# Performance work log

Hardware: AMD Instinct MI355X
Metric: run time of the kernel (lower is better)

Reference implementation:

```python
import jax, jax.numpy as jnp
import numpy as np

N_EMBD = 1024
HEAD_SIZE = 128

def setup_inputs() -> dict:
    key = jax.random.key(0)
    k1, k2, k3, k4 = jax.random.split(key, 4)
    x = jax.random.normal(k1, (8, 2048, N_EMBD), dtype=jnp.float32)
    # Linear(n_embd, head_size, bias=False): y = x @ W, W: [n_embd, head_size]
    s = 1.0 / np.sqrt(N_EMBD)
    Wk = jax.random.uniform(k2, (N_EMBD, HEAD_SIZE), jnp.float32, -s, s)
    Wq = jax.random.uniform(k3, (N_EMBD, HEAD_SIZE), jnp.float32, -s, s)
    Wv = jax.random.uniform(k4, (N_EMBD, HEAD_SIZE), jnp.float32, -s, s)
    return {"x": x, "Wk": Wk, "Wq": Wq, "Wv": Wv}

def reference(x, Wk, Wq, Wv):
    B, T, C = x.shape
    H = Wk.shape[1]
    k = jnp.einsum('btc,ch->bth', x, Wk)
    q = jnp.einsum('btc,ch->bth', x, Wq)
    v = jnp.einsum('btc,ch->bth', x, Wv)
    # scores [B, T, T], causal mask, scaled by head_size**-0.5
    wei = jnp.einsum('bqh,bkh->bqk', q, k) * (H ** -0.5)
    causal = jnp.tril(jnp.ones((T, T), dtype=bool))
    wei = jnp.where(causal, wei, -jnp.inf)
    wei = jax.nn.softmax(wei, axis=-1)
    # dropout p=0.0 (eval mode): identity
    out = jnp.einsum('bqk,bkh->bqh', wei, v)
    return out
```

## Files before the change

### kernel.cpp

```cpp
#include <hip/hip_runtime.h>
#include <hip/hip_bf16.h>
#include <stdint.h>

typedef short v8s __attribute__((ext_vector_type(8)));
typedef float v4f __attribute__((ext_vector_type(4)));
typedef float v16f __attribute__((ext_vector_type(16)));

#define N_EMBD 1024
#define HEAD 128
#define TOKENS 16384
#define T_SEQ 2048
#define BATCH 8
#define BPB 96

__device__ __forceinline__ short f2bf(float f) {
    union { float f; uint32_t u; } c; c.f = f;
    uint32_t u = c.u;
    uint32_t r = (u + 0x7fffu + ((u >> 16) & 1u)) >> 16;
    return (short)r;
}

__device__ __forceinline__ float bf2f(short s) {
    union { uint32_t u; float f; } c; c.u = ((uint32_t)(uint16_t)s) << 16;
    return c.f;
}

__device__ __forceinline__ void dma16(const void* g, void* l) {
    __builtin_amdgcn_global_load_lds(
        (const __attribute__((address_space(1))) uint32_t*)g,
        (__attribute__((address_space(3))) uint32_t*)l, 16, 0, 0);
}

__global__ __launch_bounds__(256)
void wt_kernel(const float* __restrict__ Wq, const float* __restrict__ Wk,
               const float* __restrict__ Wv, short* __restrict__ wt) {
    int tid = blockIdx.x * 256 + threadIdx.x;
    int w   = tid >> 17;
    int rem = tid & 131071;
    int c = rem >> 7, h = rem & 127;
    const float* src = (w == 0) ? Wq : ((w == 1) ? Wk : Wv);
    wt[w * 131072 + h * 1024 + c] = f2bf(src[rem]);
}

__global__ __launch_bounds__(256)
void qkv_gemm(const float* __restrict__ x, const short* __restrict__ wt,
              short* __restrict__ qkv, short* __restrict__ vT) {
    const int bid = blockIdx.x;
    const int xcd = bid & 7, q = bid >> 3;
    const int mt  = xcd * 32 + q / 3;
    const int w   = q % 3;
    const int m0  = mt * 64;

    __shared__ short smem[2][6656];

    const int t = threadIdx.x;
    const int wv = t >> 6, lane = t & 63;
    const int l31 = lane & 31, l1 = lane >> 5;
    const int wm = wv & 1, wn = wv >> 1;

    const short* wtw = wt + w * 131072;

    const int arow = t >> 3, ac4 = t & 7;
    const float* aptr0 = x + (size_t)(m0 + arow) * 1024 + ac4 * 4;
    const float* aptr1 = x + (size_t)(m0 + arow + 32) * 1024 + ac4 * 4;

    const int bc0 = (wv * 2) * 64 + lane, bc1 = (wv * 2 + 1) * 64 + lane;
    const int br0 = bc0 >> 2, bh0 = (bc0 & 3) ^ (br0 & 3);
    const int br1 = bc1 >> 2, bh1 = (bc1 & 3) ^ (br1 & 3);
    const short* bsrc0 = wtw + br0 * 1024 + bh0 * 8;
    const short* bsrc1 = wtw + br1 * 1024 + bh1 * 8;

    v16f acc[2];
    for (int i = 0; i < 16; ++i) { acc[0][i] = 0.f; acc[1][i] = 0.f; }

    {
        short* sB = smem[0] + 2560;
        dma16(bsrc0, &sB[(wv * 2) * 512]);
        dma16(bsrc1, &sB[(wv * 2 + 1) * 512]);
        float4 a0 = *(const float4*)aptr0;
        float4 a1 = *(const float4*)aptr1;
        short* sA = smem[0];
        union { short s2[4]; uint64_t u; } p0, p1;
        p0.s2[0] = f2bf(a0.x); p0.s2[1] = f2bf(a0.y); p0.s2[2] = f2bf(a0.z); p0.s2[3] = f2bf(a0.w);
        p1.s2[0] = f2bf(a1.x); p1.s2[1] = f2bf(a1.y); p1.s2[2] = f2bf(a1.z); p1.s2[3] = f2bf(a1.w);
        *(uint64_t*)&sA[arow * 40 + ac4 * 4] = p0.u;
        *(uint64_t*)&sA[(arow + 32) * 40 + ac4 * 4] = p1.u;
    }
    __syncthreads();

    float4 af0, af1;
    for (int it = 0; it < 32; ++it) {
        const int cur = it & 1, nxt = cur ^ 1;
        if (it < 31) {
            int kk = (it + 1) * 32;
            short* nB = smem[nxt] + 2560;
            dma16(bsrc0 + kk, &nB[(wv * 2) * 512]);
            dma16(bsrc1 + kk, &nB[(wv * 2 + 1) * 512]);
            af0 = *(const float4*)(aptr0 + kk);
            af1 = *(const float4*)(aptr1 + kk);
        }
        const short* sA = smem[cur];
        const short* sB = smem[cur] + 2560;
        for (int ks = 0; ks < 2; ++ks) {
            v8s a = *(const v8s*)&sA[(wm * 32 + l31) * 40 + ks * 16 + l1 * 8];
            for (int ni = 0; ni < 2; ++ni) {
                int row = wn * 64 + ni * 32 + l31;
                int sch = (ks * 2 + l1) ^ (row & 3);
                v8s b = *(const v8s*)&sB[row * 32 + sch * 8];
                acc[ni] = __builtin_amdgcn_mfma_f32_32x32x16_bf16(a, b, acc[ni], 0, 0, 0);
            }
        }
        if (it < 31) {
            short* nA = smem[nxt];
            union { short s2[4]; uint64_t u; } p0, p1;
            p0.s2[0] = f2bf(af0.x); p0.s2[1] = f2bf(af0.y); p0.s2[2] = f2bf(af0.z); p0.s2[3] = f2bf(af0.w);
            p1.s2[0] = f2bf(af1.x); p1.s2[1] = f2bf(af1.y); p1.s2[2] = f2bf(af1.z); p1.s2[3] = f2bf(af1.w);
            *(uint64_t*)&nA[arow * 40 + ac4 * 4] = p0.u;
            *(uint64_t*)&nA[(arow + 32) * 40 + ac4 * 4] = p1.u;
        }
        __syncthreads();
    }

    if (w < 2) {
        short* outw = qkv + (size_t)w * TOKENS * HEAD;
        for (int ni = 0; ni < 2; ++ni) {
            int col = wn * 64 + ni * 32 + l31;
            for (int reg = 0; reg < 16; ++reg) {
                int m = (reg & 3) + 8 * (reg >> 2) + 4 * l1;
                outw[(size_t)(m0 + wm * 32 + m) * HEAD + col] = f2bf(acc[ni][reg]);
            }
        }
    } else {
        short* sT = (short*)smem;
        for (int ni = 0; ni < 2; ++ni) {
            int col = wn * 64 + ni * 32 + l31;
            for (int g = 0; g < 4; ++g) {
                union { short s2[4]; uint64_t u; } pk;
                for (int r = 0; r < 4; ++r) pk.s2[r] = f2bf(acc[ni][g * 4 + r]);
                *(uint64_t*)&sT[col * 72 + wm * 32 + 8 * g + 4 * l1] = pk.u;
            }
        }
        __syncthreads();
        for (int it = 0; it < 4; ++it) {
            int c = it * 256 + t;
            int col = c >> 3, c8 = c & 7;
            uint4 d = *(const uint4*)(&sT[col * 72 + c8 * 8]);
            *(uint4*)(&vT[(size_t)col * TOKENS + m0 + c8 * 8]) = d;
        }
    }
}

__global__ __launch_bounds__(256)
void attn_kernel(const short* __restrict__ qb, const short* __restrict__ kb,
                 const short* __restrict__ vT, short* __restrict__ po,
                 float* __restrict__ pl) {
    const int bid = blockIdx.x;
    const int b  = bid & 7;
    const int r0 = bid >> 3;
    int qt2 = 0, c0 = 0;
    for (;;) { int sz = (2 * qt2 + 4) / 3; if (r0 < c0 + sz) break; c0 += sz; ++qt2; }
    const int s = r0 - c0;
    const int q0 = qt2 * 128;
    const int nkt = 2 * qt2 + 2;
    const int kt0 = s * 3;
    const int kt1 = (kt0 + 3 < nkt) ? (kt0 + 3) : nkt;

    __shared__ short sK[64 * 128];
    __shared__ short sV[128 * 64];
    __shared__ short sP[128 * 72];

    const int t = threadIdx.x;
    const int wv = t >> 6, lane = t & 63, ln = lane & 15, qd = lane >> 4;
    const int wrow0 = q0 + wv * 32;

    v8s qf[2][4];
    for (int qg = 0; qg < 2; ++qg) {
        const short* qrow = qb + ((size_t)(b * T_SEQ + wrow0 + qg * 16 + ln)) * HEAD;
        for (int ks = 0; ks < 4; ++ks)
            qf[qg][ks] = *(const v8s*)(qrow + ks * 32 + qd * 8);
    }

    const short* kb0 = kb + ((size_t)(b * T_SEQ + kt0 * 64)) * HEAD;
    const short* vb0 = vT + (size_t)(b * T_SEQ + kt0 * 64);
    size_t ksrc[4], vsrc[4];
    short *kdsts[4], *vdsts[4];
    for (int i = 0; i < 4; ++i) {
        int c = (wv * 4 + i) * 64 + lane;
        int krow = c >> 4, ksch = c & 15;
        int kch = (ksch & 8) | ((ksch ^ krow) & 7);
        ksrc[i] = (size_t)krow * HEAD + kch * 8;
        kdsts[i] = &sK[(wv * 4 + i) * 512];
        int dd = c >> 3, vsch = c & 7;
        int vch = (vsch ^ dd) & 7;
        vsrc[i] = (size_t)dd * TOKENS + vch * 8;
        vdsts[i] = &sV[(wv * 4 + i) * 512];
    }

    for (int i = 0; i < 4; ++i) dma16(kb0 + ksrc[i], kdsts[i]);
    for (int i = 0; i < 4; ++i) dma16(vb0 + vsrc[i], vdsts[i]);
    __syncthreads();

    v4f o[2][8] = {};
    float rs[2] = {0.f, 0.f};
    const float sc = 1.4426950408889634f / 11.313708498984761f;

    for (int kt = kt0; kt < kt1; ++kt) {
        const bool active = (kt * 64 < wrow0 + 32);
        v4f st[2][4] = {};
        if (active) {
            for (int ni = 0; ni < 4; ++ni) {
                int krow = ni * 16 + ln;
                for (int ks = 0; ks < 4; ++ks) {
                    int ch = ks * 4 + qd;
                    v8s kf = *(const v8s*)&sK[krow * 128 + ((ch & 8) | ((ch ^ krow) & 7)) * 8];
                    st[0][ni] = __builtin_amdgcn_mfma_f32_16x16x32_bf16(kf, qf[0][ks], st[0][ni], 0, 0, 0);
                    st[1][ni] = __builtin_amdgcn_mfma_f32_16x16x32_bf16(kf, qf[1][ks], st[1][ni], 0, 0, 0);
                }
            }
        }
        __syncthreads();
        if (kt + 1 < kt1) {
            const short* kbn = kb0 + (size_t)(kt + 1 - kt0) * 64 * HEAD;
            for (int i = 0; i < 4; ++i) dma16(kbn + ksrc[i], kdsts[i]);
        }

        if (active) {
            const bool needMask = (kt * 64 + 63 > wrow0);
            for (int qg = 0; qg < 2; ++qg) {
                int prow = wv * 32 + qg * 16 + ln;
                int qrow_g = wrow0 + qg * 16 + ln;
                for (int ni = 0; ni < 4; ++ni) {
                    union { short s2[4]; uint64_t u; } pk;
                    for (int r = 0; r < 4; ++r) {
                        float p = exp2f(st[qg][ni][r] * sc);
                        int kg = kt * 64 + ni * 16 + qd * 4 + r;
                        if (needMask && kg > qrow_g) p = 0.f;
                        rs[qg] += p;
                        pk.s2[r] = f2bf(p);
                    }
                    *(uint64_t*)(&sP[prow * 72 + ni * 16 + qd * 4]) = pk.u;
                }
            }
            for (int kk2 = 0; kk2 < 2; ++kk2) {
                v8s pf0 = *(const v8s*)&sP[(wv * 32 + ln) * 72 + kk2 * 32 + qd * 8];
                v8s pf1 = *(const v8s*)&sP[(wv * 32 + 16 + ln) * 72 + kk2 * 32 + qd * 8];
                for (int oni = 0; oni < 8; ++oni) {
                    int dd = oni * 16 + ln;
                    int ch = kk2 * 4 + qd;
                    v8s vf = *(const v8s*)&sV[dd * 64 + ((ch ^ dd) & 7) * 8];
                    o[0][oni] = __builtin_amdgcn_mfma_f32_16x16x32_bf16(vf, pf0, o[0][oni], 0, 0, 0);
                    o[1][oni] = __builtin_amdgcn_mfma_f32_16x16x32_bf16(vf, pf1, o[1][oni], 0, 0, 0);
                }
            }
        }
        __syncthreads();
        if (kt + 1 < kt1) {
            const short* vbn = vb0 + (kt + 1 - kt0) * 64;
            for (int i = 0; i < 4; ++i) dma16(vbn + vsrc[i], vdsts[i]);
        }
    }

    float lsum[2];
    for (int qg = 0; qg < 2; ++qg) {
        float v = rs[qg];
        v += __shfl_xor(v, 16);
        v += __shfl_xor(v, 32);
        lsum[qg] = v;
    }

    short* pob = po + (size_t)bid * 128 * 128;
    for (int qg = 0; qg < 2; ++qg)
        for (int oni = 0; oni < 8; ++oni) {
            union { short s2[4]; uint2 u; } pk;
            for (int r = 0; r < 4; ++r) pk.s2[r] = f2bf(o[qg][oni][r]);
            *(uint2*)(&pob[(((qg * 8 + oni) * 4 + wv) * 64 + lane) * 4]) = pk.u;
        }
    if (lane < 16)
        for (int qg = 0; qg < 2; ++qg)
            pl[bid * 128 + wv * 32 + qg * 16 + lane] = lsum[qg];
}

__global__ __launch_bounds__(256)
void combine_kernel(const short* __restrict__ po, const float* __restrict__ pl,
                    float* __restrict__ out) {
    const int bid = blockIdx.x;
    const int dh  = bid & 1;
    const int qh  = (bid >> 1) & 1;
    const int qt2 = (bid >> 2) & 15;
    const int b   = bid >> 6;
    int cum = 0;
    for (int j = 0; j < qt2; ++j) cum += (2 * j + 4) / 3;
    const int S = (2 * qt2 + 4) / 3;

    const int t = threadIdx.x;
    const int wv = t >> 6, lane = t & 63, ln = lane & 15, qd = lane >> 4;

    float l = 0.f;
    float accv[4][4] = {};

    for (int si = 0; si < S; ++si) {
        int slot = (cum + si) * 8 + b;
        l += pl[slot * 128 + wv * 32 + qh * 16 + ln];
        const short* pob = po + (size_t)slot * 16384;
        for (int oi = 0; oi < 4; ++oi) {
            int oni = dh * 4 + oi;
            union { short s2[4]; uint2 u; } pk;
            pk.u = *(const uint2*)(&pob[(((qh * 8 + oni) * 4 + wv) * 64 + lane) * 4]);
            for (int r = 0; r < 4; ++r) accv[oi][r] += bf2f(pk.s2[r]);
        }
    }
    float inv = 1.f / l;
    float* ob = out + ((size_t)(b * T_SEQ) + qt2 * 128 + wv * 32 + qh * 16 + ln) * HEAD;
    for (int oi = 0; oi < 4; ++oi) {
        float4 o4 = make_float4(accv[oi][0] * inv, accv[oi][1] * inv,
                                accv[oi][2] * inv, accv[oi][3] * inv);
        *(float4*)(ob + (dh * 4 + oi) * 16 + qd * 4) = o4;
    }
}

extern "C" void kernel_launch(void* const* d_in, const int* in_sizes, int n_in,
                              void* d_out, int out_size, void* d_ws, size_t ws_size,
                              hipStream_t stream) {
    const float* x  = (const float*)d_in[0];
    const float* Wk = (const float*)d_in[1];
    const float* Wq = (const float*)d_in[2];
    const float* Wv = (const float*)d_in[3];
    float* out = (float*)d_out;

    char* ws = (char*)d_ws;
    short* wt = (short*)ws;
    short* qb = (short*)(ws + 0x100000u);
    short* kb = (short*)(ws + 0x500000u);
    short* vT = (short*)(ws + 0x900000u);
    short* po = (short*)(ws + 0xD00000u);
    float* pl = (float*)(ws + 0x2500000u);
    short* qkv = qb;

    wt_kernel<<<1536, 256, 0, stream>>>(Wq, Wk, Wv, wt);
    qkv_gemm<<<768, 256, 0, stream>>>(x, wt, qkv, vT);
    attn_kernel<<<BATCH * BPB, 256, 0, stream>>>(qb, kb, vT, po, pl);
    combine_kernel<<<512, 256, 0, stream>>>(po, pl, out);
}
```

Baseline: 171.7 us.

## Tile weight transpose through LDS, reswizzle GEMM B tile, split combine finer

```diff
diff --git a/kernel.cpp b/kernel.cpp
--- a/kernel.cpp
+++ b/kernel.cpp
@@ -34,12 +34,28 @@
 __global__ __launch_bounds__(256)
 void wt_kernel(const float* __restrict__ Wq, const float* __restrict__ Wk,
                const float* __restrict__ Wv, short* __restrict__ wt) {
-    int tid = blockIdx.x * 256 + threadIdx.x;
-    int w   = tid >> 17;
-    int rem = tid & 131071;
-    int c = rem >> 7, h = rem & 127;
+    const int bid = blockIdx.x;
+    const int w = bid >> 3, c0 = (bid & 7) * 128;
     const float* src = (w == 0) ? Wq : ((w == 1) ? Wk : Wv);
-    wt[w * 131072 + h * 1024 + c] = f2bf(src[rem]);
+
+    __shared__ short sT[128 * 136];
+    const int t = threadIdx.x;
+
+    for (int i = 0; i < 16; ++i) {
+        int row = i * 8 + (t >> 5);
+        int c4  = t & 31;
+        float4 f = *(const float4*)(src + (size_t)(c0 + row) * 128 + c4 * 4);
+        sT[(c4 * 4 + 0) * 136 + row] = f2bf(f.x);
+        sT[(c4 * 4 + 1) * 136 + row] = f2bf(f.y);
+        sT[(c4 * 4 + 2) * 136 + row] = f2bf(f.z);
+        sT[(c4 * 4 + 3) * 136 + row] = f2bf(f.w);
+    }
+    __syncthreads();
+    for (int j = 0; j < 8; ++j) {
+        int h = j * 16 + (t >> 4), c8 = t & 15;
+        uint4 d = *(const uint4*)&sT[h * 136 + c8 * 8];
+        *(uint4*)&wt[w * 131072 + h * 1024 + c0 + c8 * 8] = d;
+    }
 }
 
 __global__ __launch_bounds__(256)
@@ -64,11 +80,13 @@
     const float* aptr0 = x + (size_t)(m0 + arow) * 1024 + ac4 * 4;
     const float* aptr1 = x + (size_t)(m0 + arow + 32) * 1024 + ac4 * 4;
 
-    const int bc0 = (wv * 2) * 64 + lane, bc1 = (wv * 2 + 1) * 64 + lane;
-    const int br0 = bc0 >> 2, bh0 = (bc0 & 3) ^ (br0 & 3);
-    const int br1 = bc1 >> 2, bh1 = (bc1 & 3) ^ (br1 & 3);
-    const short* bsrc0 = wtw + br0 * 1024 + bh0 * 8;
-    const short* bsrc1 = wtw + br1 * 1024 + bh1 * 8;
+    const int c0i = (wv * 2) * 64 + lane, c1i = c0i + 64;
+    const int r0 = ((c0i >> 5) << 3) | ((c0i >> 2) & 7);
+    const int j0 = (c0i & 3) ^ ((r0 >> 1) & 3);
+    const int r1 = ((c1i >> 5) << 3) | ((c1i >> 2) & 7);
+    const int j1 = (c1i & 3) ^ ((r1 >> 1) & 3);
+    const short* bsrc0 = wtw + r0 * 1024 + j0 * 8;
+    const short* bsrc1 = wtw + r1 * 1024 + j1 * 8;
 
     v16f acc[2];
     for (int i = 0; i < 16; ++i) { acc[0][i] = 0.f; acc[1][i] = 0.f; }
@@ -105,8 +123,8 @@
             v8s a = *(const v8s*)&sA[(wm * 32 + l31) * 40 + ks * 16 + l1 * 8];
             for (int ni = 0; ni < 2; ++ni) {
                 int row = wn * 64 + ni * 32 + l31;
-                int sch = (ks * 2 + l1) ^ (row & 3);
-                v8s b = *(const v8s*)&sB[row * 32 + sch * 8];
+                int a16 = ((row >> 3) << 5) | ((row & 7) << 2) | ((ks * 2 + l1) ^ ((row >> 1) & 3));
+                v8s b = *(const v8s*)&sB[a16 * 8];
                 acc[ni] = __builtin_amdgcn_mfma_f32_32x32x16_bf16(a, b, acc[ni], 0, 0, 0);
             }
         }
@@ -284,10 +302,10 @@
 void combine_kernel(const short* __restrict__ po, const float* __restrict__ pl,
                     float* __restrict__ out) {
     const int bid = blockIdx.x;
-    const int dh  = bid & 1;
-    const int qh  = (bid >> 1) & 1;
-    const int qt2 = (bid >> 2) & 15;
-    const int b   = bid >> 6;
+    const int dh  = bid & 3;
+    const int qh  = (bid >> 2) & 1;
+    const int qt2 = (bid >> 3) & 15;
+    const int b   = bid >> 7;
     int cum = 0;
     for (int j = 0; j < qt2; ++j) cum += (2 * j + 4) / 3;
     const int S = (2 * qt2 + 4) / 3;
@@ -296,14 +314,14 @@
     const int wv = t >> 6, lane = t & 63, ln = lane & 15, qd = lane >> 4;
 
     float l = 0.f;
-    float accv[4][4] = {};
+    float accv[2][4] = {};
 
     for (int si = 0; si < S; ++si) {
         int slot = (cum + si) * 8 + b;
         l += pl[slot * 128 + wv * 32 + qh * 16 + ln];
         const short* pob = po + (size_t)slot * 16384;
-        for (int oi = 0; oi < 4; ++oi) {
-            int oni = dh * 4 + oi;
+        for (int oi = 0; oi < 2; ++oi) {
+            int oni = dh * 2 + oi;
             union { short s2[4]; uint2 u; } pk;
             pk.u = *(const uint2*)(&pob[(((qh * 8 + oni) * 4 + wv) * 64 + lane) * 4]);
             for (int r = 0; r < 4; ++r) accv[oi][r] += bf2f(pk.s2[r]);
@@ -311,10 +329,10 @@
     }
     float inv = 1.f / l;
     float* ob = out + ((size_t)(b * T_SEQ) + qt2 * 128 + wv * 32 + qh * 16 + ln) * HEAD;
-    for (int oi = 0; oi < 4; ++oi) {
+    for (int oi = 0; oi < 2; ++oi) {
         float4 o4 = make_float4(accv[oi][0] * inv, accv[oi][1] * inv,
                                 accv[oi][2] * inv, accv[oi][3] * inv);
-        *(float4*)(ob + (dh * 4 + oi) * 16 + qd * 4) = o4;
+        *(float4*)(ob + (dh * 2 + oi) * 16 + qd * 4) = o4;
     }
 }
 
@@ -336,8 +354,8 @@
     float* pl = (float*)(ws + 0x2500000u);
     short* qkv = qb;
 
-    wt_kernel<<<1536, 256, 0, stream>>>(Wq, Wk, Wv, wt);
+    wt_kernel<<<24, 256, 0, stream>>>(Wq, Wk, Wv, wt);
     qkv_gemm<<<768, 256, 0, stream>>>(x, wt, qkv, vT);
     attn_kernel<<<BATCH * BPB, 256, 0, stream>>>(qb, kb, vT, po, pl);
-    combine_kernel<<<512, 256, 0, stream>>>(po, pl, out);
-}
+    combine_kernel<<<1024, 256, 0, stream>>>(po, pl, out);
+}
```

After: 176.9 us. +3.0%, slower.
